# Kernel optimization log

Measured on AMD Instinct MI355X. Metric: run time of the kernel, lower is better.

The kernel has to match this reference:

```python
import jax, jax.numpy as jnp
import numpy as np

SHAPES = ((100, 100), (50, 50), (25, 25))  # (H_l, W_l) per level
D, HEADS, HD, L, P = 256, 8, 32, 3, 4


def setup_inputs() -> dict:
    key = jax.random.key(0)
    ks = jax.random.split(key, 12)
    B = 2
    Nq = sum(h * w for h, w in SHAPES)  # 13125
    inp = {
        "query": jax.random.normal(ks[0], (B, Nq, D), jnp.float32),
        "reference_points": jax.random.uniform(ks[1], (B, Nq, L, 2), jnp.float32),
        "value0": jax.random.normal(ks[2], (B, SHAPES[0][0] * SHAPES[0][1], D), jnp.float32),
        "value1": jax.random.normal(ks[3], (B, SHAPES[1][0] * SHAPES[1][1], D), jnp.float32),
        "value2": jax.random.normal(ks[4], (B, SHAPES[2][0] * SHAPES[2][1], D), jnp.float32),
        "W_val": jax.random.normal(ks[5], (D, D), jnp.float32) * 0.05,
        "b_val": jnp.zeros((D,), jnp.float32),
        "W_off": jax.random.normal(ks[6], (D, HEADS * L * P * 2), jnp.float32) * 0.01,
        "b_off": jax.random.normal(ks[7], (HEADS * L * P * 2,), jnp.float32) * 2.0,
        "W_attn": jax.random.normal(ks[8], (D, HEADS * L * P), jnp.float32) * 0.02,
        "b_attn": jnp.zeros((HEADS * L * P,), jnp.float32),
        "W_out": jax.random.normal(ks[9], (D, D), jnp.float32) * 0.05,
        "b_out": jnp.zeros((D,), jnp.float32),
    }
    return inp


def _bilinear_sample(v, Hl, Wl, loc):
    """v: (B, heads, Hl*Wl, hd); loc: (B, Nq, heads, P, 2) normalized coords in [0,1].
    Matches torch F.grid_sample(mode='bilinear', padding_mode='zeros', align_corners=False)
    applied to grid = 2*loc - 1. Returns (B, Nq, heads, P, hd)."""
    B, heads, _, hd = v.shape
    Nq, Pn = loc.shape[1], loc.shape[3]
    # align_corners=False: pixel = ((g+1)*size - 1)/2 with g = 2*loc-1  ->  loc*size - 0.5
    x = loc[..., 0] * Wl - 0.5
    y = loc[..., 1] * Hl - 0.5
    x0 = jnp.floor(x)
    y0 = jnp.floor(y)
    wx1 = x - x0
    wy1 = y - y0
    out = jnp.zeros((B, Nq, heads, Pn, hd), v.dtype)
    for xi, wx in ((x0, 1.0 - wx1), (x0 + 1.0, wx1)):
        for yi, wy in ((y0, 1.0 - wy1), (y0 + 1.0, wy1)):
            inb = (xi >= 0) & (xi < Wl) & (yi >= 0) & (yi < Hl)
            idx = (jnp.clip(yi, 0, Hl - 1) * Wl + jnp.clip(xi, 0, Wl - 1)).astype(jnp.int32)
            idx_t = idx.transpose(0, 2, 1, 3).reshape(B, heads, Nq * Pn)  # (B,H,Nq*P)
            g = jnp.take_along_axis(v, idx_t[..., None], axis=2)  # (B,H,Nq*P,hd)
            g = g.reshape(B, heads, Nq, Pn, hd).transpose(0, 2, 1, 3, 4)
            w = (wx * wy * inb).astype(v.dtype)  # (B,Nq,heads,P)
            out = out + g * w[..., None]
    return out


def _forward(query, reference_points, values, W_val, b_val, W_off, b_off, W_attn, b_attn, W_out, b_out):
    B, Nq, _ = query.shape
    offs = (query @ W_off + b_off).reshape(B, Nq, HEADS, L, P, 2)
    attn = jax.nn.softmax((query @ W_attn + b_attn).reshape(B, Nq, HEADS, L * P), axis=-1)
    attn = attn.reshape(B, Nq, HEADS, L, P)
    out = jnp.zeros((B, Nq, HEADS, HD), query.dtype)
    for lvl, (Hl, Wl) in enumerate(SHAPES):
        # project values, split heads: (B, heads, H*W, hd)
        v = (values[lvl] @ W_val + b_val).reshape(B, Hl * Wl, HEADS, HD).transpose(0, 2, 1, 3)
        norm = jnp.array([Wl, Hl], query.dtype)
        loc = reference_points[:, :, lvl][:, :, None, None, :] + offs[:, :, :, lvl] / norm  # (B,Nq,heads,P,2)
        sampled = _bilinear_sample(v, Hl, Wl, loc)  # (B,Nq,heads,P,hd)
        out = out + jnp.einsum('bnhp,bnhpd->bnhd', attn[:, :, :, lvl], sampled)
    out = out.reshape(B, Nq, D)
    return out @ W_out + b_out  # dropout is identity at eval


def reference(query, reference_points, value0, value1, value2, W_val, b_val, W_off, b_off, W_attn, b_attn, W_out, b_out):
    return _forward(query, reference_points, (value0, value1, value2), W_val, b_val, W_off, b_off, W_attn, b_attn, W_out, b_out)
```

## Files before the change

### kernel.cpp

```cpp
#include <hip/hip_runtime.h>
#include <hip/hip_bf16.h>
#include <math.h>

#define BATCH 2
#define NQ    13125
#define MQ    26250
#define DM    256
#define NH    8
#define HDIM  32
#define NL    3
#define NP    4
#define NTOK  13125

typedef __attribute__((ext_vector_type(8))) short bf16x8;
typedef __attribute__((ext_vector_type(4))) float f32x4;

__device__ __forceinline__ short f2bf(float f) {
    unsigned u = __float_as_uint(f);
    unsigned r = (u + 0x7FFFu + ((u >> 16) & 1u)) >> 16;
    return (short)r;
}
__device__ __forceinline__ float bf2f(unsigned short u) {
    return __uint_as_float((unsigned)u << 16);
}

__device__ __forceinline__ void gld_lds16(const short* g, short* l) {
    __builtin_amdgcn_global_load_lds(
        (const __attribute__((address_space(1))) unsigned int*)g,
        (__attribute__((address_space(3))) unsigned int*)l, 16, 0, 0);
}

__global__ __launch_bounds__(256) void wprep_kernel(const float* __restrict__ Wv,
                                                    const float* __restrict__ Wo,
                                                    const float* __restrict__ Wa,
                                                    const float* __restrict__ Wu,
                                                    short* __restrict__ Wt)
{
    const int bid = blockIdx.x;
    const int w  = bid >> 8;
    const int Ns[5]   = {256, 192, 96, 256, 96};
    const int Offs[5] = {0, 65536, 114688, 163840, 139264};
    const int N = Ns[w];
    const int flat = (bid & 255) * 256 + threadIdx.x;
    const int n = flat >> 8, k = flat & 255;
    if (n >= N) return;
    if (w == 4) { Wt[139264 + n * 256 + k] = 0; return; }
    const float* W = (w == 0) ? Wv : ((w == 1) ? Wo : ((w == 2) ? Wa : Wu));
    Wt[Offs[w] + n * 256 + k] = f2bf(W[k * N + n]);
}

__global__ __launch_bounds__(256) void gemm5_kernel(const float* __restrict__ query,
                                                    const float* __restrict__ v0,
                                                    const float* __restrict__ v1,
                                                    const float* __restrict__ v2,
                                                    const short* __restrict__ Wt_val,
                                                    const short* __restrict__ Wt_off,
                                                    const float* __restrict__ b_val,
                                                    const float* __restrict__ b_off,
                                                    const float* __restrict__ b_attn,
                                                    short* __restrict__ vws,
                                                    float* __restrict__ offs,
                                                    float* __restrict__ lgts)
{
    __shared__ short As[128 * 32];
    __shared__ short Bs[128 * 32];

    const int tid  = threadIdx.x;
    const int y    = blockIdx.y;
    const int m0   = blockIdx.x * 128;
    const bool isv = (y < 2);
    const short* Wt = isv ? Wt_val : Wt_off;
    const int n0 = isv ? y * 128 : (y - 2) * 128;

    const int r  = tid >> 1;
    const int h  = tid & 1;
    const int gm = m0 + r;
    const int gmc = (gm < MQ) ? gm : (MQ - 1);
    const float* Arow;
    if (isv) {
        const int b  = gmc / NTOK;
        const int rr = gmc % NTOK;
        if (rr < 10000)      Arow = v0 + (size_t)(b * 10000 + rr) * 256;
        else if (rr < 12500) Arow = v1 + (size_t)(b * 2500 + rr - 10000) * 256;
        else                 Arow = v2 + (size_t)(b * 625 + rr - 12500) * 256;
    } else {
        Arow = query + (size_t)gmc * 256;
    }
    const int pA0 = ((h * 2 + 0) ^ ((r >> 1) & 3)) << 3;
    const int pA1 = ((h * 2 + 1) ^ ((r >> 1) & 3)) << 3;
    short* lAr = As + r * 32;

    const int row0 = tid >> 2;
    const int row1 = row0 + 64;
    const int kqs  = (tid & 3) ^ ((row0 >> 1) & 3);
    const short* gB0 = Wt + (size_t)(n0 + row0) * 256 + kqs * 8;
    const short* gB1 = Wt + (size_t)(n0 + row1) * 256 + kqs * 8;
    short* lB0 = Bs + tid * 8;
    short* lB1 = Bs + (256 + tid) * 8;

    const int lane = tid & 63;
    const int wave = tid >> 6;
    const int wm   = (wave & 1) * 64;
    const int wn   = (wave >> 1) * 64;
    const int ml   = lane & 15;
    const int kq   = lane >> 4;

    f32x4 acc[4][4] = {};

    for (int k0 = 0; k0 < 256; k0 += 32) {
        gld_lds16(gB0 + k0, lB0);
        gld_lds16(gB1 + k0, lB1);

        const float4 a0 = *(const float4*)(Arow + k0 + h * 16 + 0);
        const float4 a1 = *(const float4*)(Arow + k0 + h * 16 + 4);
        const float4 a2 = *(const float4*)(Arow + k0 + h * 16 + 8);
        const float4 a3 = *(const float4*)(Arow + k0 + h * 16 + 12);
        union { bf16x8 v; short s[8]; } t0, t1;
        t0.s[0] = f2bf(a0.x); t0.s[1] = f2bf(a0.y); t0.s[2] = f2bf(a0.z); t0.s[3] = f2bf(a0.w);
        t0.s[4] = f2bf(a1.x); t0.s[5] = f2bf(a1.y); t0.s[6] = f2bf(a1.z); t0.s[7] = f2bf(a1.w);
        t1.s[0] = f2bf(a2.x); t1.s[1] = f2bf(a2.y); t1.s[2] = f2bf(a2.z); t1.s[3] = f2bf(a2.w);
        t1.s[4] = f2bf(a3.x); t1.s[5] = f2bf(a3.y); t1.s[6] = f2bf(a3.z); t1.s[7] = f2bf(a3.w);
        *(bf16x8*)(lAr + pA0) = t0.v;
        *(bf16x8*)(lAr + pA1) = t1.v;

        __syncthreads();

        bf16x8 af[4], bfr[4];
#pragma unroll
        for (int ti = 0; ti < 4; ++ti) {
            const int rr = wm + ti * 16 + ml;
            af[ti] = *(const bf16x8*)&As[rr * 32 + ((kq ^ ((rr >> 1) & 3)) << 3)];
        }
#pragma unroll
        for (int tj = 0; tj < 4; ++tj) {
            const int rr = wn + tj * 16 + ml;
            bfr[tj] = *(const bf16x8*)&Bs[rr * 32 + ((kq ^ ((rr >> 1) & 3)) << 3)];
        }
#pragma unroll
        for (int ti = 0; ti < 4; ++ti)
#pragma unroll
            for (int tj = 0; tj < 4; ++tj)
                acc[ti][tj] = __builtin_amdgcn_mfma_f32_16x16x32_bf16(af[ti], bfr[tj], acc[ti][tj], 0, 0, 0);

        __syncthreads();
    }

#pragma unroll
    for (int tj = 0; tj < 4; ++tj) {
        const int gn = n0 + wn + tj * 16 + ml;
#pragma unroll
        for (int ti = 0; ti < 4; ++ti) {
#pragma unroll
            for (int rr = 0; rr < 4; ++rr) {
                const int gmo = m0 + wm + ti * 16 + kq * 4 + rr;
                if (gmo >= MQ) continue;
                const float v = acc[ti][tj][rr];
                if (isv) {
                    vws[(size_t)gmo * 256 + gn] = f2bf(v + b_val[gn]);
                } else {
                    if (gn < 192)      offs[(size_t)gmo * 192 + gn]        = v + b_off[gn];
                    else if (gn < 288) lgts[(size_t)gmo * 96 + (gn - 192)] = v + b_attn[gn - 192];
                }
            }
        }
    }
}

__device__ __forceinline__ void gemm_core128(const short* __restrict__ A,
                                             const short* __restrict__ Wt,
                                             int m0, int n0,
                                             f32x4 (&acc)[4][4],
                                             short* As, short* Bs)
{
    const int tid  = threadIdx.x;
    const int lane = tid & 63;
    const int wave = tid >> 6;
    const int wm   = (wave & 1) * 64;
    const int wn   = (wave >> 1) * 64;
    const int ml   = lane & 15;
    const int kq   = lane >> 4;

    const int row0 = tid >> 2;
    const int row1 = row0 + 64;
    const int kqs  = (tid & 3) ^ ((row0 >> 1) & 3);
    const short* gA0 = A  + (size_t)(m0 + row0) * 256 + kqs * 8;
    const short* gA1 = A  + (size_t)(m0 + row1) * 256 + kqs * 8;
    const short* gB0 = Wt + (size_t)(n0 + row0) * 256 + kqs * 8;
    const short* gB1 = Wt + (size_t)(n0 + row1) * 256 + kqs * 8;
    short* lA0 = As + tid * 8;
    short* lA1 = As + (256 + tid) * 8;
    short* lB0 = Bs + tid * 8;
    short* lB1 = Bs + (256 + tid) * 8;
    const bool a0ok = (m0 + row0) < MQ;
    const bool a1ok = (m0 + row1) < MQ;

    for (int k0 = 0; k0 < 256; k0 += 32) {
        if (a0ok) gld_lds16(gA0 + k0, lA0);
        if (a1ok) gld_lds16(gA1 + k0, lA1);
        gld_lds16(gB0 + k0, lB0);
        gld_lds16(gB1 + k0, lB1);
        __syncthreads();

        bf16x8 af[4], bfr[4];
#pragma unroll
        for (int ti = 0; ti < 4; ++ti) {
            const int r = wm + ti * 16 + ml;
            af[ti] = *(const bf16x8*)&As[r * 32 + ((kq ^ ((r >> 1) & 3)) << 3)];
        }
#pragma unroll
        for (int tj = 0; tj < 4; ++tj) {
            const int r = wn + tj * 16 + ml;
            bfr[tj] = *(const bf16x8*)&Bs[r * 32 + ((kq ^ ((r >> 1) & 3)) << 3)];
        }
#pragma unroll
        for (int ti = 0; ti < 4; ++ti)
#pragma unroll
            for (int tj = 0; tj < 4; ++tj)
                acc[ti][tj] = __builtin_amdgcn_mfma_f32_16x16x32_bf16(af[ti], bfr[tj], acc[ti][tj], 0, 0, 0);

        __syncthreads();
    }
}

__global__ __launch_bounds__(256) void ogemm_kernel(const short* __restrict__ A,
                                                    const short* __restrict__ Wt,
                                                    const float* __restrict__ bias,
                                                    float* __restrict__ C)
{
    __shared__ short As[128 * 32];
    __shared__ short Bs[128 * 32];
    const int m0 = blockIdx.y * 128;
    const int n0 = blockIdx.x * 128;

    f32x4 acc[4][4] = {};
    gemm_core128(A, Wt, m0, n0, acc, As, Bs);

    const int tid  = threadIdx.x;
    const int lane = tid & 63;
    const int wave = tid >> 6;
    const int wm   = (wave & 1) * 64;
    const int wn   = (wave >> 1) * 64;
    const int ml   = lane & 15;
    const int kq   = lane >> 4;

#pragma unroll
    for (int tj = 0; tj < 4; ++tj) {
        const int gn = n0 + wn + tj * 16 + ml;
#pragma unroll
        for (int ti = 0; ti < 4; ++ti) {
#pragma unroll
            for (int r = 0; r < 4; ++r) {
                const int gm = m0 + wm + ti * 16 + kq * 4 + r;
                if (gm >= MQ) continue;
                C[(size_t)gm * 256 + gn] = acc[ti][tj][r] + bias[gn];
            }
        }
    }
}

__global__ __launch_bounds__(256) void sample_kernel(const short* __restrict__ vws,
                                                     const float* __restrict__ offs,
                                                     const float* __restrict__ logits,
                                                     const float* __restrict__ refp,
                                                     short* __restrict__ mid)
{
    const int q0  = blockIdx.x * 4;
    const int tid = threadIdx.x;

    __shared__ float  s_lg[4][96];
    __shared__ float  s_ref[4][6];
    __shared__ float  s_stat[4][NH][2];
    __shared__ float4 s_w[4][96];
    __shared__ int4   s_i[4][96];

    for (int idx = tid; idx < 384; idx += 256) {
        const int qq = idx / 96, s = idx % 96;
        const int q = q0 + qq;
        if (q < MQ) s_lg[qq][s] = logits[(size_t)q * 96 + s];
    }
    if (tid < 24) {
        const int qq = tid / 6, j = tid % 6;
        const int q = q0 + qq;
        if (q < MQ) s_ref[qq][j] = refp[(size_t)q * 6 + j];
    }
    __syncthreads();

    if (tid < 32) {
        const int qq = tid >> 3, h = tid & 7;
        if (q0 + qq < MQ) {
            float mx = -1e30f;
#pragma unroll
            for (int i = 0; i < 12; ++i) mx = fmaxf(mx, s_lg[qq][h * 12 + i]);
            float ssum = 0.f;
#pragma unroll
            for (int i = 0; i < 12; ++i) ssum += expf(s_lg[qq][h * 12 + i] - mx);
            s_stat[qq][h][0] = mx;
            s_stat[qq][h][1] = 1.f / ssum;
        }
    }
    __syncthreads();

    for (int idx = tid; idx < 384; idx += 256) {
        const int qq = idx / 96, s = idx % 96;
        const int q  = q0 + qq;
        if (q >= MQ) continue;
        const int b  = q / NQ;
        const int h  = s / 12, i = s % 12;
        const int l  = i >> 2, p = i & 3;

        const int Hs[3] = {100, 50, 25};
        const int Wz[3] = {100, 50, 25};
        const int Lo[3] = {0, 10000, 12500};
        const int Wl = Wz[l], Hl = Hs[l];
        const float fW = (float)Wl, fH = (float)Hl;

        const float aw = expf(s_lg[qq][s] - s_stat[qq][h][0]) * s_stat[qq][h][1];

        const int oi = (((h * NL) + l) * NP + p) * 2;
        const float2 offp = *(const float2*)(offs + (size_t)q * 192 + oi);
        const float rx = s_ref[qq][l * 2 + 0];
        const float ry = s_ref[qq][l * 2 + 1];

        const float x = (rx + offp.x / fW) * fW - 0.5f;
        const float y = (ry + offp.y / fH) * fH - 0.5f;
        const float x0f = floorf(x), y0f = floorf(y);
        const int   x0 = (int)x0f,  y0 = (int)y0f;
        const float wx1 = x - x0f, wy1 = y - y0f;
        const float wx0 = 1.f - wx1, wy0 = 1.f - wy1;

        const bool xin0 = (x0 >= 0) && (x0 < Wl);
        const bool xin1 = (x0 + 1 >= 0) && (x0 + 1 < Wl);
        const bool yin0 = (y0 >= 0) && (y0 < Hl);
        const bool yin1 = (y0 + 1 >= 0) && (y0 + 1 < Hl);

        const int cx0 = min(max(x0, 0), Wl - 1);
        const int cx1 = min(max(x0 + 1, 0), Wl - 1);
        const int cy0 = min(max(y0, 0), Hl - 1);
        const int cy1 = min(max(y0 + 1, 0), Hl - 1);

        const int base = b * NTOK + Lo[l];
        int4 idxv;
        idxv.x = base + cy0 * Wl + cx0;
        idxv.y = base + cy0 * Wl + cx1;
        idxv.z = base + cy1 * Wl + cx0;
        idxv.w = base + cy1 * Wl + cx1;

        float4 w;
        w.x = (xin0 && yin0) ? aw * wx0 * wy0 : 0.f;
        w.y = (xin1 && yin0) ? aw * wx1 * wy0 : 0.f;
        w.z = (xin0 && yin1) ? aw * wx0 * wy1 : 0.f;
        w.w = (xin1 && yin1) ? aw * wx1 * wy1 : 0.f;

        s_w[qq][s] = w;
        s_i[qq][s] = idxv;
    }
    __syncthreads();

    {
        const int qq = tid >> 6;
        const int q  = q0 + qq;
        if (q < MQ) {
            const int r  = tid & 63;
            const int h  = r >> 3;
            const int c4 = (r & 7) * 4;
            const int ch = h * HDIM + c4;

            float a0 = 0.f, a1 = 0.f, a2 = 0.f, a3 = 0.f;
#pragma unroll
            for (int s = 0; s < 12; ++s) {
                const float4 w  = s_w[qq][h * 12 + s];
                const int4   id = s_i[qq][h * 12 + s];
                const ushort4 u0 = *(const ushort4*)(vws + (size_t)id.x * DM + ch);
                const ushort4 u1 = *(const ushort4*)(vws + (size_t)id.y * DM + ch);
                const ushort4 u2 = *(const ushort4*)(vws + (size_t)id.z * DM + ch);
                const ushort4 u3 = *(const ushort4*)(vws + (size_t)id.w * DM + ch);
                a0 += w.x * bf2f(u0.x) + w.y * bf2f(u1.x) + w.z * bf2f(u2.x) + w.w * bf2f(u3.x);
                a1 += w.x * bf2f(u0.y) + w.y * bf2f(u1.y) + w.z * bf2f(u2.y) + w.w * bf2f(u3.y);
                a2 += w.x * bf2f(u0.z) + w.y * bf2f(u1.z) + w.z * bf2f(u2.z) + w.w * bf2f(u3.z);
                a3 += w.x * bf2f(u0.w) + w.y * bf2f(u1.w) + w.z * bf2f(u2.w) + w.w * bf2f(u3.w);
            }
            short4 o;
            o.x = f2bf(a0); o.y = f2bf(a1); o.z = f2bf(a2); o.w = f2bf(a3);
            *(short4*)(mid + (size_t)q * DM + ch) = o;
        }
    }
}

extern "C" void kernel_launch(void* const* d_in, const int* in_sizes, int n_in,
                              void* d_out, int out_size, void* d_ws, size_t ws_size,
                              hipStream_t stream)
{
    const float* query  = (const float*)d_in[0];
    const float* refp   = (const float*)d_in[1];
    const float* v0     = (const float*)d_in[2];
    const float* v1     = (const float*)d_in[3];
    const float* v2     = (const float*)d_in[4];
    const float* W_val  = (const float*)d_in[5];
    const float* b_val  = (const float*)d_in[6];
    const float* W_off  = (const float*)d_in[7];
    const float* b_off  = (const float*)d_in[8];
    const float* W_attn = (const float*)d_in[9];
    const float* b_attn = (const float*)d_in[10];
    const float* W_out  = (const float*)d_in[11];
    const float* b_out  = (const float*)d_in[12];
    float* out = (float*)d_out;

    float* ws   = (float*)d_ws;
    float* offs = ws;
    float* lgts = offs + (size_t)MQ * 192;
    short* vws  = (short*)(lgts + (size_t)MQ * 96);
    short* mid  = vws + (size_t)MQ * DM;
    short* Wt   = mid + (size_t)MQ * DM;
    short* Wt_val = Wt;
    short* Wt_off = Wt + 65536;
    short* Wt_out = Wt + 163840;

    wprep_kernel<<<1280, 256, 0, stream>>>(W_val, W_off, W_attn, W_out, Wt);
    {
        dim3 grid((MQ + 127) / 128, 5);
        gemm5_kernel<<<grid, 256, 0, stream>>>(query, v0, v1, v2, Wt_val, Wt_off,
                                               b_val, b_off, b_attn, vws, offs, lgts);
    }
    sample_kernel<<<(MQ + 3) / 4, 256, 0, stream>>>(vws, offs, lgts, refp, mid);
    {
        dim3 grid(2, (MQ + 127) / 128);
        ogemm_kernel<<<grid, 256, 0, stream>>>(mid, Wt_out, b_out, out);
    }
}
```

Measured before the change: 228.3 us.

## Widen sampling gathers to 16B, pack FMAs, use hardware bf16 pack conversion

The sampling kernel now handles 8 queries per block, with each thread gathering 8 bf16 channels per corner through 16-byte loads instead of 4. It accumulates with packed v_pk_fma_f32, stores precomputed element offsets, and uses fast __expf. Both the GEMM A-tile conversion and the sampling output use the v_cvt_pk_bf16_f32 instruction instead of manual rounding. The aim is fewer memory transactions and fewer ALU instructions in the gather-bound sampling stage. Half as many threads now cover each query, which lowers memory-level parallelism per query. Results may also differ slightly because of __expf and the hardware rounding mode.

```diff
diff --git a/kernel.cpp b/kernel.cpp
--- a/kernel.cpp
+++ b/kernel.cpp
@@ -14,6 +14,7 @@
 
 typedef __attribute__((ext_vector_type(8))) short bf16x8;
 typedef __attribute__((ext_vector_type(4))) float f32x4;
+typedef __attribute__((ext_vector_type(2))) float f32x2;
 
 __device__ __forceinline__ short f2bf(float f) {
     unsigned u = __float_as_uint(f);
@@ -22,6 +23,11 @@
 }
 __device__ __forceinline__ float bf2f(unsigned short u) {
     return __uint_as_float((unsigned)u << 16);
+}
+__device__ __forceinline__ unsigned cvt_pk_bf16(float lo, float hi) {
+    unsigned r;
+    asm("v_cvt_pk_bf16_f32 %0, %1, %2" : "=v"(r) : "v"(lo), "v"(hi));
+    return r;
 }
 
 __device__ __forceinline__ void gld_lds16(const short* g, short* l) {
@@ -115,11 +121,11 @@
         const float4 a1 = *(const float4*)(Arow + k0 + h * 16 + 4);
         const float4 a2 = *(const float4*)(Arow + k0 + h * 16 + 8);
         const float4 a3 = *(const float4*)(Arow + k0 + h * 16 + 12);
-        union { bf16x8 v; short s[8]; } t0, t1;
-        t0.s[0] = f2bf(a0.x); t0.s[1] = f2bf(a0.y); t0.s[2] = f2bf(a0.z); t0.s[3] = f2bf(a0.w);
-        t0.s[4] = f2bf(a1.x); t0.s[5] = f2bf(a1.y); t0.s[6] = f2bf(a1.z); t0.s[7] = f2bf(a1.w);
-        t1.s[0] = f2bf(a2.x); t1.s[1] = f2bf(a2.y); t1.s[2] = f2bf(a2.z); t1.s[3] = f2bf(a2.w);
-        t1.s[4] = f2bf(a3.x); t1.s[5] = f2bf(a3.y); t1.s[6] = f2bf(a3.z); t1.s[7] = f2bf(a3.w);
+        union { bf16x8 v; unsigned u[4]; } t0, t1;
+        t0.u[0] = cvt_pk_bf16(a0.x, a0.y); t0.u[1] = cvt_pk_bf16(a0.z, a0.w);
+        t0.u[2] = cvt_pk_bf16(a1.x, a1.y); t0.u[3] = cvt_pk_bf16(a1.z, a1.w);
+        t1.u[0] = cvt_pk_bf16(a2.x, a2.y); t1.u[1] = cvt_pk_bf16(a2.z, a2.w);
+        t1.u[2] = cvt_pk_bf16(a3.x, a3.y); t1.u[3] = cvt_pk_bf16(a3.z, a3.w);
         *(bf16x8*)(lAr + pA0) = t0.v;
         *(bf16x8*)(lAr + pA1) = t1.v;
 
@@ -258,34 +264,46 @@
     }
 }
 
+__device__ __forceinline__ void pk_acc(f32x2 (&acc)[4], uint4 u, float w) {
+    f32x2 w2 = {w, w};
+    unsigned ud[4] = {u.x, u.y, u.z, u.w};
+#pragma unroll
+    for (int d = 0; d < 4; ++d) {
+        f32x2 v2;
+        v2.x = __uint_as_float(ud[d] << 16);
+        v2.y = __uint_as_float(ud[d] & 0xFFFF0000u);
+        asm("v_pk_fma_f32 %0, %1, %2, %0" : "+v"(acc[d]) : "v"(v2), "v"(w2));
+    }
+}
+
 __global__ __launch_bounds__(256) void sample_kernel(const short* __restrict__ vws,
                                                      const float* __restrict__ offs,
                                                      const float* __restrict__ logits,
                                                      const float* __restrict__ refp,
                                                      short* __restrict__ mid)
 {
-    const int q0  = blockIdx.x * 4;
+    const int q0  = blockIdx.x * 8;
     const int tid = threadIdx.x;
 
-    __shared__ float  s_lg[4][96];
-    __shared__ float  s_ref[4][6];
-    __shared__ float  s_stat[4][NH][2];
-    __shared__ float4 s_w[4][96];
-    __shared__ int4   s_i[4][96];
-
-    for (int idx = tid; idx < 384; idx += 256) {
+    __shared__ float  s_lg[8][96];
+    __shared__ float  s_ref[8][6];
+    __shared__ float  s_stat[8][NH][2];
+    __shared__ float4 s_w[8][96];
+    __shared__ int4   s_i[8][96];
+
+    for (int idx = tid; idx < 768; idx += 256) {
         const int qq = idx / 96, s = idx % 96;
         const int q = q0 + qq;
         if (q < MQ) s_lg[qq][s] = logits[(size_t)q * 96 + s];
     }
-    if (tid < 24) {
+    if (tid < 48) {
         const int qq = tid / 6, j = tid % 6;
         const int q = q0 + qq;
         if (q < MQ) s_ref[qq][j] = refp[(size_t)q * 6 + j];
     }
     __syncthreads();
 
-    if (tid < 32) {
+    if (tid < 64) {
         const int qq = tid >> 3, h = tid & 7;
         if (q0 + qq < MQ) {
             float mx = -1e30f;
@@ -293,14 +311,14 @@
             for (int i = 0; i < 12; ++i) mx = fmaxf(mx, s_lg[qq][h * 12 + i]);
             float ssum = 0.f;
 #pragma unroll
-            for (int i = 0; i < 12; ++i) ssum += expf(s_lg[qq][h * 12 + i] - mx);
+            for (int i = 0; i < 12; ++i) ssum += __expf(s_lg[qq][h * 12 + i] - mx);
             s_stat[qq][h][0] = mx;
             s_stat[qq][h][1] = 1.f / ssum;
         }
     }
     __syncthreads();
 
-    for (int idx = tid; idx < 384; idx += 256) {
+    for (int idx = tid; idx < 768; idx += 256) {
         const int qq = idx / 96, s = idx % 96;
         const int q  = q0 + qq;
         if (q >= MQ) continue;
@@ -314,7 +332,7 @@
         const int Wl = Wz[l], Hl = Hs[l];
         const float fW = (float)Wl, fH = (float)Hl;
 
-        const float aw = expf(s_lg[qq][s] - s_stat[qq][h][0]) * s_stat[qq][h][1];
+        const float aw = __expf(s_lg[qq][s] - s_stat[qq][h][0]) * s_stat[qq][h][1];
 
         const int oi = (((h * NL) + l) * NP + p) * 2;
         const float2 offp = *(const float2*)(offs + (size_t)q * 192 + oi);
@@ -340,10 +358,10 @@
 
         const int base = b * NTOK + Lo[l];
         int4 idxv;
-        idxv.x = base + cy0 * Wl + cx0;
-        idxv.y = base + cy0 * Wl + cx1;
-        idxv.z = base + cy1 * Wl + cx0;
-        idxv.w = base + cy1 * Wl + cx1;
+        idxv.x = (base + cy0 * Wl + cx0) << 8;
+        idxv.y = (base + cy0 * Wl + cx1) << 8;
+        idxv.z = (base + cy1 * Wl + cx0) << 8;
+        idxv.w = (base + cy1 * Wl + cx1) << 8;
 
         float4 w;
         w.x = (xin0 && yin0) ? aw * wx0 * wy0 : 0.f;
@@ -351,37 +369,41 @@
         w.z = (xin0 && yin1) ? aw * wx0 * wy1 : 0.f;
         w.w = (xin1 && yin1) ? aw * wx1 * wy1 : 0.f;
 
-        s_w[qq][s] = w;
-        s_i[qq][s] = idxv;
+        const int slot = i * 8 + h;
+        s_w[qq][slot] = w;
+        s_i[qq][slot] = idxv;
     }
     __syncthreads();
 
     {
-        const int qq = tid >> 6;
+        const int qq = tid >> 5;
         const int q  = q0 + qq;
         if (q < MQ) {
-            const int r  = tid & 63;
-            const int h  = r >> 3;
-            const int c4 = (r & 7) * 4;
-            const int ch = h * HDIM + c4;
-
-            float a0 = 0.f, a1 = 0.f, a2 = 0.f, a3 = 0.f;
+            const int r   = tid & 31;
+            const int h   = r >> 2;
+            const int chb = h * HDIM + (r & 3) * 8;
+
+            f32x2 acc[4] = {};
 #pragma unroll
             for (int s = 0; s < 12; ++s) {
-                const float4 w  = s_w[qq][h * 12 + s];
-                const int4   id = s_i[qq][h * 12 + s];
-                const ushort4 u0 = *(const ushort4*)(vws + (size_t)id.x * DM + ch);
-                const ushort4 u1 = *(const ushort4*)(vws + (size_t)id.y * DM + ch);
-                const ushort4 u2 = *(const ushort4*)(vws + (size_t)id.z * DM + ch);
-                const ushort4 u3 = *(const ushort4*)(vws + (size_t)id.w * DM + ch);
-                a0 += w.x * bf2f(u0.x) + w.y * bf2f(u1.x) + w.z * bf2f(u2.x) + w.w * bf2f(u3.x);
-                a1 += w.x * bf2f(u0.y) + w.y * bf2f(u1.y) + w.z * bf2f(u2.y) + w.w * bf2f(u3.y);
-                a2 += w.x * bf2f(u0.z) + w.y * bf2f(u1.z) + w.z * bf2f(u2.z) + w.w * bf2f(u3.z);
-                a3 += w.x * bf2f(u0.w) + w.y * bf2f(u1.w) + w.z * bf2f(u2.w) + w.w * bf2f(u3.w);
+                const int slot = s * 8 + h;
+                const float4 w  = s_w[qq][slot];
+                const int4   id = s_i[qq][slot];
+                const uint4 u0 = *(const uint4*)(vws + id.x + chb);
+                const uint4 u1 = *(const uint4*)(vws + id.y + chb);
+                const uint4 u2 = *(const uint4*)(vws + id.z + chb);
+                const uint4 u3 = *(const uint4*)(vws + id.w + chb);
+                pk_acc(acc, u0, w.x);
+                pk_acc(acc, u1, w.y);
+                pk_acc(acc, u2, w.z);
+                pk_acc(acc, u3, w.w);
             }
-            short4 o;
-            o.x = f2bf(a0); o.y = f2bf(a1); o.z = f2bf(a2); o.w = f2bf(a3);
-            *(short4*)(mid + (size_t)q * DM + ch) = o;
+            uint4 o;
+            o.x = cvt_pk_bf16(acc[0].x, acc[0].y);
+            o.y = cvt_pk_bf16(acc[1].x, acc[1].y);
+            o.z = cvt_pk_bf16(acc[2].x, acc[2].y);
+            o.w = cvt_pk_bf16(acc[3].x, acc[3].y);
+            *(uint4*)(mid + (size_t)q * DM + chb) = o;
         }
     }
 }
@@ -421,7 +443,7 @@
         gemm5_kernel<<<grid, 256, 0, stream>>>(query, v0, v1, v2, Wt_val, Wt_off,
                                                b_val, b_off, b_attn, vws, offs, lgts);
     }
-    sample_kernel<<<(MQ + 3) / 4, 256, 0, stream>>>(vws, offs, lgts, refp, mid);
+    sample_kernel<<<(MQ + 7) / 8, 256, 0, stream>>>(vws, offs, lgts, refp, mid);
     {
         dim3 grid(2, (MQ + 127) / 128);
         ogemm_kernel<<<grid, 256, 0, stream>>>(mid, Wt_out, b_out, out);
```

After: 227.2 us. No clear change (-0.5%).
